# Kernel tuning notes

Measured on AMD Instinct MI355X. Metric: run time of the kernel, lower is better.

## Reference

```python
import jax, jax.numpy as jnp
import numpy as np

ALPHA = 0.7
BETTA = 0.3
EPS = 1e-8


def _unit(v):
    n = jnp.linalg.norm(v, axis=-1, keepdims=True)
    return v / jnp.where(n > 0, n, 1.0)


def setup_inputs() -> dict:
    key = jax.random.key(0)
    k1, k2 = jax.random.split(key)
    N, D = 2097152, 3
    vec_1 = jax.random.normal(k1, (N, D), dtype=jnp.float32)
    vec_2 = jax.random.normal(k2, (N, D), dtype=jnp.float32)
    return {"vec_1": vec_1, "vec_2": vec_2}


def reference(vec_1, vec_2):
    # Row mask: keep rows where ||vec_1|| > 1e-8. Instead of boolean gather
    # (data-dependent shape), weight rows by the mask and divide by the count.
    norm1 = jnp.linalg.norm(vec_1, axis=-1, keepdims=True)  # [N,1]
    mask = (norm1 > EPS).astype(vec_1.dtype)                # [N,1]

    n1 = _unit(vec_1)                                       # [N,3]
    u2 = _unit(vec_2)
    # angle between vec_1 and vec_2 (RotationVectors.angle)
    cos_sim = jnp.clip(jnp.sum(n1 * u2, axis=-1), -1.0, 1.0)  # [N]
    a = jnp.arccos(cos_sim)
    # orthonormal companion: Gram-Schmidt of vec_2 against n1
    n2 = _unit(vec_2 - n1 * jnp.sum(n1 * vec_2, axis=-1, keepdims=True))

    sin_a = jnp.sin(a)[:, None]            # [N,1]
    cos_a_m1 = (jnp.cos(a) - 1.0)[:, None]  # [N,1]

    # bmm(M, ones) is just the row-sum of M. For M = x yT the row-sum is
    # x * sum(y), so we never materialize the [N,3,3] outer products:
    s1 = jnp.sum(n1, axis=-1, keepdims=True)  # [N,1]
    s2 = jnp.sum(n2, axis=-1, keepdims=True)
    u_ta = sin_a * (n2 * s1 - n1 * s2)        # transform_a @ ones, [N,3]
    u_tb = cos_a_m1 * (n1 * s1 + n2 * s2)     # transform_b @ ones, [N,3]
    # I @ ones == ones, so mse(I@ones, ones) == 0 elementwise.
    per_row = ALPHA * u_ta ** 2 + BETTA * u_tb ** 2  # [N,3]

    cnt = jnp.maximum(jnp.sum(mask), 1.0)
    loss = jnp.sum(per_row * mask, axis=0) / cnt     # mean over kept rows -> [3]
    return jnp.nan_to_num(loss, nan=0.0, posinf=0.1, neginf=-0.1)
```

## Files before the change

kernel.cpp:

```cpp
#include <hip/hip_runtime.h>
#include <math.h>

#define ALPHA 0.7f
#define BETTA 0.3f
#define EPS   1e-8f

#define BLOCK 64
#define RPT   4
#define TILE_ROWS (BLOCK * RPT)
#define TILE_F4   (TILE_ROWS * 3 / 4)
#define TILE_DW   (TILE_ROWS * 3)
#define LDS_DW    (TILE_DW + TILE_DW / 12)

__device__ __forceinline__ void row_contrib(float x1, float y1, float z1,
                                            float x2, float y2, float z2,
                                            float& a0, float& a1, float& a2,
                                            float& ac) {
    float q1 = x1 * x1 + y1 * y1 + z1 * z1;
    float m = (q1 > EPS * EPS) ? 1.0f : 0.0f;
    float inv1 = (q1 > 0.0f) ? rsqrtf(q1) : 0.0f;
    float n1x = x1 * inv1, n1y = y1 * inv1, n1z = z1 * inv1;

    float q2 = x2 * x2 + y2 * y2 + z2 * z2;
    float inv2 = (q2 > 0.0f) ? rsqrtf(q2) : 0.0f;
    float u2x = x2 * inv2, u2y = y2 * inv2, u2z = z2 * inv2;

    float c = n1x * u2x + n1y * u2y + n1z * u2z;
    c = fminf(1.0f, fmaxf(-1.0f, c));
    float sin_a = sqrtf(fmaxf(0.0f, 1.0f - c * c));
    float cm1 = c - 1.0f;

    float d = n1x * x2 + n1y * y2 + n1z * z2;
    float wx = x2 - n1x * d, wy = y2 - n1y * d, wz = z2 - n1z * d;
    float wq = wx * wx + wy * wy + wz * wz;
    float invw = (wq > 0.0f) ? rsqrtf(wq) : 0.0f;
    float n2x = wx * invw, n2y = wy * invw, n2z = wz * invw;

    float s1 = n1x + n1y + n1z;
    float s2 = n2x + n2y + n2z;

    float tax = sin_a * (n2x * s1 - n1x * s2);
    float tay = sin_a * (n2y * s1 - n1y * s2);
    float taz = sin_a * (n2z * s1 - n1z * s2);

    float tbx = cm1 * (n1x * s1 + n2x * s2);
    float tby = cm1 * (n1y * s1 + n2y * s2);
    float tbz = cm1 * (n1z * s1 + n2z * s2);

    a0 += (ALPHA * tax * tax + BETTA * tbx * tbx) * m;
    a1 += (ALPHA * tay * tay + BETTA * tby * tby) * m;
    a2 += (ALPHA * taz * taz + BETTA * tbz * tbz) * m;
    ac += m;
}

__device__ __forceinline__ void lds_store_f4(float* lds, int L0, float4 v) {
    int q = L0 / 12;
    int p = L0 + q;
    lds[p + 0] = v.x;
    lds[p + 1] = v.y;
    lds[p + 2] = v.z;
    lds[p + 3] = v.w;
}

__global__ __launch_bounds__(BLOCK) void trl_reduce(const float* __restrict__ v1,
                                                    const float* __restrict__ v2,
                                                    float4* __restrict__ ws,
                                                    int n_rows, int n_tiles) {
    __shared__ float ldsA[LDS_DW];
    __shared__ float ldsB[LDS_DW];

    int t = threadIdx.x;
    float a0 = 0.0f, a1 = 0.0f, a2 = 0.0f, ac = 0.0f;

    if (blockIdx.x < (unsigned)n_tiles) {
        const float4* g1 = (const float4*)v1;
        const float4* g2 = (const float4*)v2;
        long base = (long)blockIdx.x * TILE_F4;

        float4 la0 = g1[base + 0 * BLOCK + t];
        float4 la1 = g1[base + 1 * BLOCK + t];
        float4 la2 = g1[base + 2 * BLOCK + t];
        float4 lb0 = g2[base + 0 * BLOCK + t];
        float4 lb1 = g2[base + 1 * BLOCK + t];
        float4 lb2 = g2[base + 2 * BLOCK + t];

        int u = 4 * t;
        lds_store_f4(ldsA, 0 * 256 + u, la0);
        lds_store_f4(ldsA, 1 * 256 + u, la1);
        lds_store_f4(ldsA, 2 * 256 + u, la2);
        lds_store_f4(ldsB, 0 * 256 + u, lb0);
        lds_store_f4(ldsB, 1 * 256 + u, lb1);
        lds_store_f4(ldsB, 2 * 256 + u, lb2);
        __syncthreads();

        float fA[12], fB[12];
        int rb = 13 * t;
#pragma unroll
        for (int k = 0; k < 12; ++k) fA[k] = ldsA[rb + k];
#pragma unroll
        for (int k = 0; k < 12; ++k) fB[k] = ldsB[rb + k];

        row_contrib(fA[0], fA[1], fA[2],  fB[0], fB[1], fB[2],  a0, a1, a2, ac);
        row_contrib(fA[3], fA[4], fA[5],  fB[3], fB[4], fB[5],  a0, a1, a2, ac);
        row_contrib(fA[6], fA[7], fA[8],  fB[6], fB[7], fB[8],  a0, a1, a2, ac);
        row_contrib(fA[9], fA[10], fA[11], fB[9], fB[10], fB[11], a0, a1, a2, ac);
    }

    if (blockIdx.x == 0) {
        for (long r = (long)n_tiles * TILE_ROWS + t; r < n_rows; r += BLOCK) {
            const float* q1 = v1 + r * 3;
            const float* q2 = v2 + r * 3;
            row_contrib(q1[0], q1[1], q1[2], q2[0], q2[1], q2[2], a0, a1, a2, ac);
        }
    }

    for (int off = 32; off > 0; off >>= 1) {
        a0 += __shfl_down(a0, off, 64);
        a1 += __shfl_down(a1, off, 64);
        a2 += __shfl_down(a2, off, 64);
        ac += __shfl_down(ac, off, 64);
    }
    if (t == 0) {
        float4 o;
        o.x = a0; o.y = a1; o.z = a2; o.w = ac;
        ws[blockIdx.x] = o;
    }
}

__global__ __launch_bounds__(256) void trl_final(const float4* __restrict__ ws,
                                                 float* __restrict__ out,
                                                 int nblocks) {
    float s0 = 0.0f, s1 = 0.0f, s2 = 0.0f, sc = 0.0f;
    for (int i = threadIdx.x; i < nblocks; i += 256) {
        float4 p = ws[i];
        s0 += p.x; s1 += p.y; s2 += p.z; sc += p.w;
    }
    for (int off = 32; off > 0; off >>= 1) {
        s0 += __shfl_down(s0, off, 64);
        s1 += __shfl_down(s1, off, 64);
        s2 += __shfl_down(s2, off, 64);
        sc += __shfl_down(sc, off, 64);
    }
    __shared__ float smem[4][4];
    int lane = threadIdx.x & 63;
    int wave = threadIdx.x >> 6;
    if (lane == 0) {
        smem[wave][0] = s0;
        smem[wave][1] = s1;
        smem[wave][2] = s2;
        smem[wave][3] = sc;
    }
    __syncthreads();
    if (threadIdx.x < 3) {
        float num = smem[0][threadIdx.x] + smem[1][threadIdx.x] +
                    smem[2][threadIdx.x] + smem[3][threadIdx.x];
        float cnt = smem[0][3] + smem[1][3] + smem[2][3] + smem[3][3];
        cnt = fmaxf(cnt, 1.0f);
        float v = num / cnt;
        if (isnan(v)) v = 0.0f;
        else if (isinf(v)) v = (v > 0.0f) ? 0.1f : -0.1f;
        out[threadIdx.x] = v;
    }
}

extern "C" void kernel_launch(void* const* d_in, const int* in_sizes, int n_in,
                              void* d_out, int out_size, void* d_ws, size_t ws_size,
                              hipStream_t stream) {
    const float* v1 = (const float*)d_in[0];
    const float* v2 = (const float*)d_in[1];
    float* out = (float*)d_out;
    float4* ws = (float4*)d_ws;

    int n_rows = in_sizes[0] / 3;
    int n_tiles = n_rows / TILE_ROWS;
    int grid = (n_tiles > 0) ? n_tiles : 1;

    trl_reduce<<<grid, BLOCK, 0, stream>>>(v1, v2, ws, n_rows, n_tiles);
    trl_final<<<1, 256, 0, stream>>>(ws, out, grid);
}
```

Baseline: 94.43 us.

## Use 256-thread blocks with single reused LDS buffer and per-wave partials

Raises the block size from one wave to four waves, so each block handles 1024 rows and the grid shrinks fourfold. The two LDS staging buffers are merged into one that is reused for vec_1 and then vec_2, with extra barriers between the phases to keep LDS size per block bounded. Each wave writes its own partial sum to the workspace, and the final kernel reduces four times as many partials. The aim is fewer, larger blocks and lower launch/scheduling overhead, at the cost of two added __syncthreads per block and serialised LDS staging.

After: 94.93 us. About the same (+0.5%).

```diff
diff --git a/kernel.cpp b/kernel.cpp
--- a/kernel.cpp
+++ b/kernel.cpp
@@ -5,7 +5,7 @@
 #define BETTA 0.3f
 #define EPS   1e-8f
 
-#define BLOCK 64
+#define BLOCK 256
 #define RPT   4
 #define TILE_ROWS (BLOCK * RPT)
 #define TILE_F4   (TILE_ROWS * 3 / 4)
@@ -66,8 +66,7 @@
                                                     const float* __restrict__ v2,
                                                     float4* __restrict__ ws,
                                                     int n_rows, int n_tiles) {
-    __shared__ float ldsA[LDS_DW];
-    __shared__ float ldsB[LDS_DW];
+    __shared__ float lds[LDS_DW];
 
     int t = threadIdx.x;
     float a0 = 0.0f, a1 = 0.0f, a2 = 0.0f, ac = 0.0f;
@@ -85,20 +84,24 @@
         float4 lb2 = g2[base + 2 * BLOCK + t];
 
         int u = 4 * t;
-        lds_store_f4(ldsA, 0 * 256 + u, la0);
-        lds_store_f4(ldsA, 1 * 256 + u, la1);
-        lds_store_f4(ldsA, 2 * 256 + u, la2);
-        lds_store_f4(ldsB, 0 * 256 + u, lb0);
-        lds_store_f4(ldsB, 1 * 256 + u, lb1);
-        lds_store_f4(ldsB, 2 * 256 + u, lb2);
+
+        lds_store_f4(lds, 0 * 1024 + u, la0);
+        lds_store_f4(lds, 1 * 1024 + u, la1);
+        lds_store_f4(lds, 2 * 1024 + u, la2);
         __syncthreads();
 
         float fA[12], fB[12];
         int rb = 13 * t;
 #pragma unroll
-        for (int k = 0; k < 12; ++k) fA[k] = ldsA[rb + k];
+        for (int k = 0; k < 12; ++k) fA[k] = lds[rb + k];
+        __syncthreads();
+
+        lds_store_f4(lds, 0 * 1024 + u, lb0);
+        lds_store_f4(lds, 1 * 1024 + u, lb1);
+        lds_store_f4(lds, 2 * 1024 + u, lb2);
+        __syncthreads();
 #pragma unroll
-        for (int k = 0; k < 12; ++k) fB[k] = ldsB[rb + k];
+        for (int k = 0; k < 12; ++k) fB[k] = lds[rb + k];
 
         row_contrib(fA[0], fA[1], fA[2],  fB[0], fB[1], fB[2],  a0, a1, a2, ac);
         row_contrib(fA[3], fA[4], fA[5],  fB[3], fB[4], fB[5],  a0, a1, a2, ac);
@@ -120,18 +123,20 @@
         a2 += __shfl_down(a2, off, 64);
         ac += __shfl_down(ac, off, 64);
     }
-    if (t == 0) {
+    int lane = t & 63;
+    int wave = t >> 6;
+    if (lane == 0) {
         float4 o;
         o.x = a0; o.y = a1; o.z = a2; o.w = ac;
-        ws[blockIdx.x] = o;
+        ws[(size_t)blockIdx.x * 4 + wave] = o;
     }
 }
 
 __global__ __launch_bounds__(256) void trl_final(const float4* __restrict__ ws,
                                                  float* __restrict__ out,
-                                                 int nblocks) {
+                                                 int nparts) {
     float s0 = 0.0f, s1 = 0.0f, s2 = 0.0f, sc = 0.0f;
-    for (int i = threadIdx.x; i < nblocks; i += 256) {
+    for (int i = threadIdx.x; i < nparts; i += 256) {
         float4 p = ws[i];
         s0 += p.x; s1 += p.y; s2 += p.z; sc += p.w;
     }
@@ -176,5 +181,5 @@
     int grid = (n_tiles > 0) ? n_tiles : 1;
 
     trl_reduce<<<grid, BLOCK, 0, stream>>>(v1, v2, ws, n_rows, n_tiles);
-    trl_final<<<1, 256, 0, stream>>>(ws, out, grid);
+    trl_final<<<1, 256, 0, stream>>>(ws, out, grid * 4);
 }
```
